# Optimization experiments

Hardware: AMD Instinct MI355X
Metric: run time of the kernel (lower is better)

## Reference

```python
import jax, jax.numpy as jnp
import numpy as np

NY, NX = 2048, 2048
DX = 5.0
DT = 0.8
BETA = 4.0
RHO = 1.0 / 9.81
EPS_ETA = 0.001
MANNING2 = 0.055 ** 2
PAD = ((0, 0), (0, 0), (1, 1), (1, 1))


def _conv3(x, w):
    # 1-channel 3x3 stencil, VALID padding: [1,1,H+2,W+2] -> [1,1,H,W]
    return jax.lax.conv_general_dilated(
        x, w, window_strides=(1, 1), padding='VALID',
        dimension_numbers=('NCHW', 'OIHW', 'NCHW'))


def _bc_u(u):
    # zero left/right columns, copy top/bottom rows (free-slip in y, no-flow in x)
    p = jnp.pad(u, PAD)
    p = p.at[:, :, 0, :].set(p[:, :, 1, :])
    p = p.at[:, :, -1, :].set(p[:, :, -2, :])
    return p


def _bc_v(v):
    # copy left/right columns, zero top/bottom rows
    p = jnp.pad(v, PAD)
    p = p.at[:, :, :, 0].set(p[:, :, :, 1])
    p = p.at[:, :, :, -1].set(p[:, :, :, -2])
    return p


def _bc_eta(h):
    # Neumann (copy) on all four sides; column copies first, then rows (matches torch order)
    p = jnp.pad(h, PAD)
    p = p.at[:, :, :, -1].set(p[:, :, :, -2])
    p = p.at[:, :, :, 0].set(p[:, :, :, 1])
    p = p.at[:, :, -1, :].set(p[:, :, -2, :])
    p = p.at[:, :, 0, :].set(p[:, :, 1, :])
    return p


def _k_pg(wpad, u, v, w1, w2, w3):
    # Petrov-Galerkin dissipation coefficient
    amp = 0.5 * (jnp.abs(u) + jnp.abs(v)) / DX  # = 1/2 dx^-2 (|u|dx + |v|dx)
    num = 0.25 * DX * jnp.abs(amp * _conv3(wpad, w1))
    den = EPS_ETA + 0.5 * (jnp.abs(_conv3(wpad, w2)) + jnp.abs(_conv3(wpad, w3))) / DX ** 2
    return num / den


def _pg_vector(uu, vv, u, v, k3, w1, w2, w3):
    k_u = _k_pg(uu, u, v, w1, w2, w3)
    k_v = _k_pg(vv, u, v, w1, w2, w3)
    k_uu = jnp.pad(jnp.minimum(k_u, k3), PAD)
    k_vv = jnp.pad(jnp.minimum(k_v, k3), PAD)
    k_x = 0.5 * (k_u * _conv3(uu, w1) + _conv3(uu * k_uu, w1) - u * _conv3(k_uu, w1))
    k_y = 0.5 * (k_v * _conv3(vv, w1) + _conv3(vv * k_vv, w1) - v * _conv3(k_vv, w1))
    return k_x, k_y


def _pg_scalar(hh, h, u, v, k3, w1, w2, w3):
    k_u = _k_pg(hh, u, v, w1, w2, w3)
    k_uu = jnp.pad(jnp.minimum(k_u, k3), PAD)
    return 0.5 * (k_u * _conv3(hh, w1) + _conv3(hh * k_uu, w1) - h * _conv3(k_uu, w1))


def _forward(values_u, values_v, values_H, values_h, k1, k2, k3,
             source_h, dif_values_h, values_hh, w1, w2, w3, wm):
    diag = -w1[0, 0, 1, 1]
    uu = _bc_u(values_u)
    vv = _bc_v(values_v)
    k_x, k_y = _pg_vector(uu, vv, values_u, values_v, k3, w1, w2, w3)
    hp = _bc_eta(values_h)
    # predictor (half) step
    b_u = (k_x * DT - values_u * _conv3(uu, w2) * DT - values_v * _conv3(uu, w3) * DT) * 0.5 + values_u
    b_v = (k_y * DT - values_u * _conv3(vv, w2) * DT - values_v * _conv3(vv, w3) * DT) * 0.5 + values_v
    b_u = b_u - _conv3(hp, w2) * DT
    b_v = b_v - _conv3(hp, w3) * DT
    b_uu = _bc_u(b_u)  # note: padded fields built BEFORE friction division, as in source
    b_vv = _bc_v(b_v)
    depth43 = jnp.maximum(k1, values_H + values_h) ** (4.0 / 3.0)
    sigma_q = jnp.sqrt(b_u ** 2 + b_v ** 2) * MANNING2 / depth43
    b_u = b_u / (1.0 + sigma_q * DT / RHO)
    b_v = b_v / (1.0 + sigma_q * DT / RHO)
    # corrector (full) step
    k_x, k_y = _pg_vector(b_uu, b_vv, b_u, b_v, k3, w1, w2, w3)
    u_n = values_u + k_x * DT - b_u * _conv3(b_uu, w2) * DT - b_v * _conv3(b_uu, w3) * DT
    v_n = values_v + k_y * DT - b_u * _conv3(b_vv, w2) * DT - b_v * _conv3(b_vv, w3) * DT
    u_n = u_n - _conv3(hp, w2) * DT
    v_n = v_n - _conv3(hp, w3) * DT
    sigma_q = jnp.sqrt(u_n ** 2 + v_n ** 2) * MANNING2 / depth43
    u_n = u_n / (1.0 + sigma_q * DT / RHO)
    v_n = v_n / (1.0 + sigma_q * DT / RHO)
    uu = _bc_u(u_n)
    vv = _bc_v(v_n)
    eta1 = jnp.maximum(k2, values_H + values_h)
    eta2 = jnp.maximum(k1, values_H + values_h)
    e1p = _bc_eta(eta1)
    b = BETA * RHO * (
        -_conv3(e1p, w2) * u_n - _conv3(e1p, w3) * v_n
        - eta1 * _conv3(uu, w2) - eta1 * _conv3(vv, w3)
        + _pg_scalar(e1p, eta1, u_n, v_n, k3, w1, w2, w3)
        - _conv3(_bc_eta(dif_values_h), wm) / DT
        + source_h) / (DT * eta2)
    # two Jacobi iterations for the wave (pressure) equation
    coef = BETA * RHO / (DT ** 2 * eta2)
    denom = diag + coef
    hh = values_hh
    for _ in range(2):
        hh = hh - (-_conv3(_bc_eta(hh), w1) + coef * hh) / denom + b / denom
    h_new = values_h + hh
    dif_h = h_new - values_h
    hhp = _bc_eta(hh)
    u_n = u_n - _conv3(hhp, w2) * DT / RHO
    v_n = v_n - _conv3(hhp, w3) * DT / RHO
    return (u_n, v_n, h_new, hh, b, dif_h)


def setup_inputs() -> dict:
    key = jax.random.key(0)
    k = jax.random.split(key, 6)
    shape = (1, 1, NY, NX)
    w1 = jnp.asarray(np.array([[1, 1, 1], [1, -8, 1], [1, 1, 1]], np.float32) / 3.0 / DX ** 2).reshape(1, 1, 3, 3)
    w2 = jnp.asarray(np.array([[-1, 0, 1], [-4, 0, 4], [-1, 0, 1]], np.float32) / 12.0 / DX).reshape(1, 1, 3, 3)
    w3 = jnp.transpose(w2, (0, 1, 3, 2))
    wm = jnp.asarray(np.array([[1, 4, 1], [4, 16, 4], [1, 4, 1]], np.float32) / 36.0).reshape(1, 1, 3, 3)
    return {
        'values_u': jax.random.normal(k[0], shape, jnp.float32) * 0.5,
        'values_v': jax.random.normal(k[1], shape, jnp.float32) * 0.5,
        'values_H': jax.random.uniform(k[2], shape, jnp.float32) * 10.0,  # bathymetric depth
        'values_h': jax.random.normal(k[3], shape, jnp.float32) * 0.1,   # free-surface elevation
        'k1': jnp.full(shape, EPS_ETA, jnp.float32),
        'k2': jnp.zeros(shape, jnp.float32),
        'k3': jnp.full(shape, DX ** 2 * 0.1 / DT, jnp.float32),
        'source_h': jax.random.normal(k[4], shape, jnp.float32) * 0.01,
        'dif_values_h': jax.random.normal(k[5], shape, jnp.float32) * 0.01,
        'values_hh': jnp.zeros(shape, jnp.float32),
        'w1': w1, 'w2': w2, 'w3': w3, 'wm': wm,
    }


def reference(values_u, values_v, values_H, values_h, k1, k2, k3,
              source_h, dif_values_h, values_hh, w1, w2, w3, wm):
    return _forward(values_u, values_v, values_H, values_h, k1, k2, k3,
                    source_h, dif_values_h, values_hh, w1, w2, w3, wm)
```

## Files before the change

kernel.cpp:

```cpp
#include <hip/hip_runtime.h>
#include <math.h>


#define NY 2048
#define NX 2048

#define BX 32
#define BY 8
#define SW (BX + 4)
#define KW (BX + 2)

#define DXf   5.0f
#define DTf   0.8f
#define EPSf  0.001f
#define K3f   3.125f
__device__ __constant__ float M2f   = (float)(0.055 * 0.055);
__device__ __constant__ float RHOf  = (float)(1.0 / 9.81);
__device__ __constant__ float BRf   = (float)(4.0 / 9.81);
__device__ __constant__ float DT2f  = (float)(0.8 * 0.8);
__device__ __constant__ float C43f  = (float)(4.0 / 3.0);

#define W1E ((1.0f / 3.0f) / 25.0f)
#define W1C ((-8.0f / 3.0f) / 25.0f)
#define DIAGf ((8.0f / 3.0f) / 25.0f)
#define W2A ((1.0f / 12.0f) / 5.0f)
#define W2B ((4.0f / 12.0f) / 5.0f)
#define WMA (1.0f / 36.0f)
#define WMB (4.0f / 36.0f)
#define WMC (16.0f / 36.0f)

__device__ __forceinline__ int iclamp(int v, int lo, int hi) {
    return v < lo ? lo : (v > hi ? hi : v);
}

__device__ __forceinline__ float uuAt(const float* __restrict__ u, int y, int x) {
    if ((unsigned)x >= (unsigned)NX) return 0.0f;
    y = iclamp(y, 0, NY - 1);
    return u[y * NX + x];
}
__device__ __forceinline__ float vvAt(const float* __restrict__ v, int y, int x) {
    if ((unsigned)y >= (unsigned)NY) return 0.0f;
    x = iclamp(x, 0, NX - 1);
    return v[y * NX + x];
}
__device__ __forceinline__ float etaAt(const float* __restrict__ h, int y, int x) {
    y = iclamp(y, 0, NY - 1);
    x = iclamp(x, 0, NX - 1);
    return h[y * NX + x];
}

__device__ __forceinline__ float cW1(const float* s, int st) {
    float nb = s[-st - 1] + s[-st] + s[-st + 1] + s[-1] + s[1] + s[st - 1] + s[st] + s[st + 1];
    return W1E * nb + W1C * s[0];
}
__device__ __forceinline__ float cW2(const float* s, int st) {
    return W2A * ((s[-st + 1] - s[-st - 1]) + (s[st + 1] - s[st - 1])) + W2B * (s[1] - s[-1]);
}
__device__ __forceinline__ float cW3(const float* s, int st) {
    return W2A * ((s[st - 1] - s[-st - 1]) + (s[st + 1] - s[-st + 1])) + W2B * (s[st] - s[-st]);
}

__device__ __forceinline__ float kpg(float uq, float vq, float c1, float c2, float c3) {
    float amp = (0.5f * (fabsf(uq) + fabsf(vq))) / DXf;
    float num = 1.25f * fabsf(amp * c1);
    float den = EPSf + (0.5f * (fabsf(c2) + fabsf(c3))) / 25.0f;
    return num / den;
}

__device__ __forceinline__ float prodW1(const float* pf, const float* pk) {
    float nb = pf[-SW - 1] * pk[-KW - 1] + pf[-SW] * pk[-KW] + pf[-SW + 1] * pk[-KW + 1]
             + pf[-1] * pk[-1] + pf[1] * pk[1]
             + pf[SW - 1] * pk[KW - 1] + pf[SW] * pk[KW] + pf[SW + 1] * pk[KW + 1];
    return W1E * nb + W1C * (pf[0] * pk[0]);
}

__global__ __launch_bounds__(256)
void kA(const float* __restrict__ u, const float* __restrict__ v,
        const float* __restrict__ H, const float* __restrict__ h,
        float* __restrict__ bupre, float* __restrict__ bvpre,
        float* __restrict__ d43o, float* __restrict__ buo, float* __restrict__ bvo)
{
    const int tx0 = blockIdx.x * BX, ty0 = blockIdx.y * BY;
    const int lx = threadIdx.x, ly = threadIdx.y, tid = ly * BX + lx;
    __shared__ float su[BY + 4][SW], sv[BY + 4][SW], sh[BY + 2][KW];
    __shared__ float sku[BY + 2][KW], skum[BY + 2][KW], skv[BY + 2][KW], skvm[BY + 2][KW];

    for (int t = tid; t < (BY + 4) * SW; t += 256) {
        int r = t / SW, c = t % SW;
        int gy = ty0 + r - 2, gx = tx0 + c - 2;
        su[r][c] = uuAt(u, gy, gx);
        sv[r][c] = vvAt(v, gy, gx);
    }
    for (int t = tid; t < (BY + 2) * KW; t += 256) {
        int r = t / KW, c = t % KW;
        sh[r][c] = etaAt(h, ty0 + r - 1, tx0 + c - 1);
    }
    __syncthreads();

    for (int t = tid; t < (BY + 2) * KW; t += 256) {
        int r = t / KW, c = t % KW;
        int gy = ty0 + r - 1, gx = tx0 + c - 1;
        float ku = 0.f, kum = 0.f, kv = 0.f, kvm = 0.f;
        if ((unsigned)gy < (unsigned)NY && (unsigned)gx < (unsigned)NX) {
            const float* pu = &su[r + 1][c + 1];
            const float* pv = &sv[r + 1][c + 1];
            float uq = pu[0], vq = pv[0];
            ku = kpg(uq, vq, cW1(pu, SW), cW2(pu, SW), cW3(pu, SW));
            kum = fminf(ku, K3f);
            kv = kpg(uq, vq, cW1(pv, SW), cW2(pv, SW), cW3(pv, SW));
            kvm = fminf(kv, K3f);
        }
        sku[r][c] = ku; skum[r][c] = kum; skv[r][c] = kv; skvm[r][c] = kvm;
    }
    __syncthreads();

    const int y = ty0 + ly, x = tx0 + lx, idx = y * NX + x;
    const float* pu = &su[ly + 2][lx + 2];
    const float* pv = &sv[ly + 2][lx + 2];
    const float* ph = &sh[ly + 1][lx + 1];
    const float* pum = &skum[ly + 1][lx + 1];
    const float* pvm = &skvm[ly + 1][lx + 1];
    float uc = pu[0], vc = pv[0];

    float kx = 0.5f * (sku[ly + 1][lx + 1] * cW1(pu, SW) + prodW1(pu, pum) - uc * cW1(pum, KW));
    float ky = 0.5f * (skv[ly + 1][lx + 1] * cW1(pv, SW) + prodW1(pv, pvm) - vc * cW1(pvm, KW));

    float cw2u = cW2(pu, SW), cw3u = cW3(pu, SW);
    float cw2v = cW2(pv, SW), cw3v = cW3(pv, SW);
    float cw2h = cW2(ph, KW), cw3h = cW3(ph, KW);

    float bu = (kx * DTf - uc * cw2u * DTf - vc * cw3u * DTf) * 0.5f + uc;
    bu = bu - cw2h * DTf;
    float bv = (ky * DTf - uc * cw2v * DTf - vc * cw3v * DTf) * 0.5f + vc;
    bv = bv - cw3h * DTf;

    float dep = fmaxf(EPSf, H[idx] + ph[0]);
    float d43 = powf(dep, C43f);
    float sq = sqrtf(bu * bu + bv * bv) * M2f / d43;
    float fr = 1.0f + (sq * DTf) / RHOf;

    bupre[idx] = bu;
    bvpre[idx] = bv;
    d43o[idx] = d43;
    buo[idx] = bu / fr;
    bvo[idx] = bv / fr;
}

__global__ __launch_bounds__(256)
void kB(const float* __restrict__ u, const float* __restrict__ v, const float* __restrict__ h,
        const float* __restrict__ bupre, const float* __restrict__ bvpre,
        const float* __restrict__ bupost, const float* __restrict__ bvpost,
        const float* __restrict__ d43, float* __restrict__ uno, float* __restrict__ vno)
{
    const int tx0 = blockIdx.x * BX, ty0 = blockIdx.y * BY;
    const int lx = threadIdx.x, ly = threadIdx.y, tid = ly * BX + lx;
    __shared__ float su[BY + 4][SW], sv[BY + 4][SW], sh[BY + 2][KW];
    __shared__ float sku[BY + 2][KW], skum[BY + 2][KW], skv[BY + 2][KW], skvm[BY + 2][KW];

    for (int t = tid; t < (BY + 4) * SW; t += 256) {
        int r = t / SW, c = t % SW;
        int gy = ty0 + r - 2, gx = tx0 + c - 2;
        su[r][c] = uuAt(bupre, gy, gx);
        sv[r][c] = vvAt(bvpre, gy, gx);
    }
    for (int t = tid; t < (BY + 2) * KW; t += 256) {
        int r = t / KW, c = t % KW;
        sh[r][c] = etaAt(h, ty0 + r - 1, tx0 + c - 1);
    }
    __syncthreads();

    for (int t = tid; t < (BY + 2) * KW; t += 256) {
        int r = t / KW, c = t % KW;
        int gy = ty0 + r - 1, gx = tx0 + c - 1;
        float ku = 0.f, kum = 0.f, kv = 0.f, kvm = 0.f;
        if ((unsigned)gy < (unsigned)NY && (unsigned)gx < (unsigned)NX) {
            const float* pu = &su[r + 1][c + 1];
            const float* pv = &sv[r + 1][c + 1];
            float uq = bupost[gy * NX + gx], vq = bvpost[gy * NX + gx];
            ku = kpg(uq, vq, cW1(pu, SW), cW2(pu, SW), cW3(pu, SW));
            kum = fminf(ku, K3f);
            kv = kpg(uq, vq, cW1(pv, SW), cW2(pv, SW), cW3(pv, SW));
            kvm = fminf(kv, K3f);
        }
        sku[r][c] = ku; skum[r][c] = kum; skv[r][c] = kv; skvm[r][c] = kvm;
    }
    __syncthreads();

    const int y = ty0 + ly, x = tx0 + lx, idx = y * NX + x;
    const float* pu = &su[ly + 2][lx + 2];
    const float* pv = &sv[ly + 2][lx + 2];
    const float* ph = &sh[ly + 1][lx + 1];
    const float* pum = &skum[ly + 1][lx + 1];
    const float* pvm = &skvm[ly + 1][lx + 1];
    float buc = bupost[idx], bvc = bvpost[idx];

    float kx = 0.5f * (sku[ly + 1][lx + 1] * cW1(pu, SW) + prodW1(pu, pum) - buc * cW1(pum, KW));
    float ky = 0.5f * (skv[ly + 1][lx + 1] * cW1(pv, SW) + prodW1(pv, pvm) - bvc * cW1(pvm, KW));

    float un = u[idx] + kx * DTf - buc * cW2(pu, SW) * DTf - bvc * cW3(pu, SW) * DTf;
    un = un - cW2(ph, KW) * DTf;
    float vn = v[idx] + ky * DTf - buc * cW2(pv, SW) * DTf - bvc * cW3(pv, SW) * DTf;
    vn = vn - cW3(ph, KW) * DTf;

    float d = d43[idx];
    float sq = sqrtf(un * un + vn * vn) * M2f / d;
    float fr = 1.0f + (sq * DTf) / RHOf;
    uno[idx] = un / fr;
    vno[idx] = vn / fr;
}

__global__ __launch_bounds__(256)
void kC(const float* __restrict__ H, const float* __restrict__ h,
        const float* __restrict__ un, const float* __restrict__ vn,
        const float* __restrict__ dif, const float* __restrict__ src,
        const float* __restrict__ hh0,
        float* __restrict__ bo, float* __restrict__ hh1o)
{
    const int tx0 = blockIdx.x * BX, ty0 = blockIdx.y * BY;
    const int lx = threadIdx.x, ly = threadIdx.y, tid = ly * BX + lx;
    __shared__ float se[BY + 4][SW], sh0[BY + 2][KW];
    __shared__ float sks[BY + 2][KW], sksm[BY + 2][KW];

    for (int t = tid; t < (BY + 4) * SW; t += 256) {
        int r = t / SW, c = t % SW;
        int cy = iclamp(ty0 + r - 2, 0, NY - 1), cx = iclamp(tx0 + c - 2, 0, NX - 1);
        se[r][c] = fmaxf(0.0f, H[cy * NX + cx] + h[cy * NX + cx]);
    }
    for (int t = tid; t < (BY + 2) * KW; t += 256) {
        int r = t / KW, c = t % KW;
        sh0[r][c] = etaAt(hh0, ty0 + r - 1, tx0 + c - 1);
    }
    __syncthreads();

    for (int t = tid; t < (BY + 2) * KW; t += 256) {
        int r = t / KW, c = t % KW;
        int gy = ty0 + r - 1, gx = tx0 + c - 1;
        float ks = 0.f, ksm = 0.f;
        if ((unsigned)gy < (unsigned)NY && (unsigned)gx < (unsigned)NX) {
            const float* pe = &se[r + 1][c + 1];
            float uq = un[gy * NX + gx], vq = vn[gy * NX + gx];
            ks = kpg(uq, vq, cW1(pe, SW), cW2(pe, SW), cW3(pe, SW));
            ksm = fminf(ks, K3f);
        }
        sks[r][c] = ks; sksm[r][c] = ksm;
    }
    __syncthreads();

    const int y = ty0 + ly, x = tx0 + lx, idx = y * NX + x;
    const float* pe = &se[ly + 2][lx + 2];
    const float* pk = &sksm[ly + 1][lx + 1];
    float e1c = pe[0];

    float pg = 0.5f * (sks[ly + 1][lx + 1] * cW1(pe, SW) + prodW1(pe, pk) - e1c * cW1(pk, KW));
    float cw2e = cW2(pe, SW), cw3e = cW3(pe, SW);
    float unc = un[idx], vnc = vn[idx];

    float cw2un = W2A * ((uuAt(un, y - 1, x + 1) - uuAt(un, y - 1, x - 1))
                       + (uuAt(un, y + 1, x + 1) - uuAt(un, y + 1, x - 1)))
                + W2B * (uuAt(un, y, x + 1) - uuAt(un, y, x - 1));
    float cw3vn = W2A * ((vvAt(vn, y + 1, x - 1) - vvAt(vn, y - 1, x - 1))
                       + (vvAt(vn, y + 1, x + 1) - vvAt(vn, y - 1, x + 1)))
                + W2B * (vvAt(vn, y + 1, x) - vvAt(vn, y - 1, x));
    float cwm = WMA * (etaAt(dif, y - 1, x - 1) + etaAt(dif, y - 1, x + 1)
                     + etaAt(dif, y + 1, x - 1) + etaAt(dif, y + 1, x + 1))
              + WMB * (etaAt(dif, y - 1, x) + etaAt(dif, y, x - 1)
                     + etaAt(dif, y, x + 1) + etaAt(dif, y + 1, x))
              + WMC * etaAt(dif, y, x);

    float eta2 = fmaxf(EPSf, H[idx] + h[idx]);
    float sum = -cw2e * unc - cw3e * vnc - e1c * cw2un - e1c * cw3vn + pg
                - cwm / DTf + src[idx];
    float b = (BRf * sum) / (DTf * eta2);
    float coef = BRf / (DT2f * eta2);
    float dn = DIAGf + coef;

    const float* p0 = &sh0[ly + 1][lx + 1];
    float hc = p0[0];
    float cv = cW1(p0, KW);
    float hh1 = hc - (-cv + coef * hc) / dn + b / dn;

    bo[idx] = b;
    hh1o[idx] = hh1;
}

__global__ __launch_bounds__(256)
void kD(const float* __restrict__ H, const float* __restrict__ h,
        const float* __restrict__ un, const float* __restrict__ vn,
        const float* __restrict__ b, const float* __restrict__ hh1,
        float* __restrict__ o_u, float* __restrict__ o_v, float* __restrict__ o_h,
        float* __restrict__ o_hh, float* __restrict__ o_dif)
{
    const int tx0 = blockIdx.x * BX, ty0 = blockIdx.y * BY;
    const int lx = threadIdx.x, ly = threadIdx.y, tid = ly * BX + lx;
    __shared__ float s1[BY + 4][SW];
    __shared__ float s2[BY + 2][KW];

    for (int t = tid; t < (BY + 4) * SW; t += 256) {
        int r = t / SW, c = t % SW;
        s1[r][c] = etaAt(hh1, ty0 + r - 2, tx0 + c - 2);
    }
    __syncthreads();

    for (int t = tid; t < (BY + 2) * KW; t += 256) {
        int r = t / KW, c = t % KW;
        int cy = iclamp(ty0 + r - 1, 0, NY - 1), cx = iclamp(tx0 + c - 1, 0, NX - 1);
        const float* p = &s1[cy - ty0 + 2][cx - tx0 + 2];
        float hc = p[0];
        float cv = cW1(p, SW);
        int gi = cy * NX + cx;
        float coef = BRf / (DT2f * fmaxf(EPSf, H[gi] + h[gi]));
        float dn = DIAGf + coef;
        s2[r][c] = hc - (-cv + coef * hc) / dn + b[gi] / dn;
    }
    __syncthreads();

    const int y = ty0 + ly, x = tx0 + lx, idx = y * NX + x;
    const float* p2 = &s2[ly + 1][lx + 1];
    float hh2 = p2[0];
    float hcen = h[idx];
    float hnew = hcen + hh2;

    float cw2 = cW2(p2, KW), cw3 = cW3(p2, KW);

    o_u[idx] = un[idx] - (cw2 * DTf) / RHOf;
    o_v[idx] = vn[idx] - (cw3 * DTf) / RHOf;
    o_h[idx] = hnew;
    o_hh[idx] = hh2;
    o_dif[idx] = hnew - hcen;
}

extern "C" void kernel_launch(void* const* d_in, const int* in_sizes, int n_in,
                              void* d_out, int out_size, void* d_ws, size_t ws_size,
                              hipStream_t stream)
{
    const float* u   = (const float*)d_in[0];
    const float* v   = (const float*)d_in[1];
    const float* H   = (const float*)d_in[2];
    const float* h   = (const float*)d_in[3];
    const float* src = (const float*)d_in[7];
    const float* dif = (const float*)d_in[8];
    const float* hh0 = (const float*)d_in[9];

    float* out = (float*)d_out;
    const size_t N = (size_t)NY * NX;
    float* o0 = out;
    float* o1 = out + N;
    float* o2 = out + 2 * N;
    float* o3 = out + 3 * N;
    float* o4 = out + 4 * N;
    float* o5 = out + 5 * N;

    float* ws  = (float*)d_ws;
    float* un  = ws;
    float* vn  = ws + N;
    float* hh1 = ws + 2 * N;

    dim3 blk(BX, BY);
    dim3 grd(NX / BX, NY / BY);

    kA<<<grd, blk, 0, stream>>>(u, v, H, h, o0, o1, o2, o3, o4);
    kB<<<grd, blk, 0, stream>>>(u, v, h, o0, o1, o3, o4, o2, un, vn);
    kC<<<grd, blk, 0, stream>>>(H, h, un, vn, dif, src, hh0, o4, hh1);
    kD<<<grd, blk, 0, stream>>>(H, h, un, vn, o4, hh1, o0, o1, o2, o3, o5);
}
```

Measured before the change: 423.3 us.

## Widen tiles, cache stencil results in shared memory, use fast reciprocal math

Tile width doubles to 64 (512 threads per block), and halo loads become 2D strided loops with no integer division. The first-pass stencil results (cW1/cW2/cW3) are stored in shared memory so the second pass reuses them instead of recomputing. In kC, the un/vn/dif neighbourhoods are staged through shared memory rather than read from global memory nine times each. Divisions, powf and sqrtf are replaced with AMD rcp/log/exp2/sqrt intrinsics plus one Newton step, which can change precision slightly and raises shared memory use per block.

```diff
diff --git a/kernel.cpp b/kernel.cpp
--- a/kernel.cpp
+++ b/kernel.cpp
@@ -5,20 +5,26 @@
 #define NY 2048
 #define NX 2048
 
-#define BX 32
+#define BX 64
 #define BY 8
-#define SW (BX + 4)
+#define TH (BY + 4)
+#define TW (BX + 4)
+#define KH (BY + 2)
 #define KW (BX + 2)
 
 #define DXf   5.0f
 #define DTf   0.8f
 #define EPSf  0.001f
 #define K3f   3.125f
-__device__ __constant__ float M2f   = (float)(0.055 * 0.055);
-__device__ __constant__ float RHOf  = (float)(1.0 / 9.81);
-__device__ __constant__ float BRf   = (float)(4.0 / 9.81);
-__device__ __constant__ float DT2f  = (float)(0.8 * 0.8);
-__device__ __constant__ float C43f  = (float)(4.0 / 3.0);
+
+__device__ constexpr float M2f    = (float)(0.055 * 0.055);
+__device__ constexpr float RHO_   = (float)(1.0 / 9.81);
+__device__ constexpr float BRf    = (float)(4.0 / 9.81);
+__device__ constexpr float DT2f   = (float)(0.8 * 0.8);
+__device__ constexpr float C43f   = (float)(4.0 / 3.0);
+__device__ constexpr float DTRHO  = 0.8f / RHO_;
+__device__ constexpr float INVDT  = 1.0f / 0.8f;
+__device__ constexpr float CBRDT2 = BRf / DT2f;
 
 #define W1E ((1.0f / 3.0f) / 25.0f)
 #define W1C ((-8.0f / 3.0f) / 25.0f)
@@ -33,6 +39,11 @@
     return v < lo ? lo : (v > hi ? hi : v);
 }
 
+__device__ __forceinline__ float frcp(float x) {
+    float r = __builtin_amdgcn_rcpf(x);
+    return r * (2.0f - x * r);
+}
+
 __device__ __forceinline__ float uuAt(const float* __restrict__ u, int y, int x) {
     if ((unsigned)x >= (unsigned)NX) return 0.0f;
     y = iclamp(y, 0, NY - 1);
@@ -49,68 +60,86 @@
     return h[y * NX + x];
 }
 
-__device__ __forceinline__ float cW1(const float* s, int st) {
-    float nb = s[-st - 1] + s[-st] + s[-st + 1] + s[-1] + s[1] + s[st - 1] + s[st] + s[st + 1];
+template<int ST>
+__device__ __forceinline__ float cw1f(const float* s) {
+    float nb = s[-ST - 1] + s[-ST] + s[-ST + 1] + s[-1] + s[1] + s[ST - 1] + s[ST] + s[ST + 1];
     return W1E * nb + W1C * s[0];
 }
-__device__ __forceinline__ float cW2(const float* s, int st) {
-    return W2A * ((s[-st + 1] - s[-st - 1]) + (s[st + 1] - s[st - 1])) + W2B * (s[1] - s[-1]);
-}
-__device__ __forceinline__ float cW3(const float* s, int st) {
-    return W2A * ((s[st - 1] - s[-st - 1]) + (s[st + 1] - s[-st + 1])) + W2B * (s[st] - s[-st]);
-}
-
-__device__ __forceinline__ float kpg(float uq, float vq, float c1, float c2, float c3) {
-    float amp = (0.5f * (fabsf(uq) + fabsf(vq))) / DXf;
+template<int ST>
+__device__ __forceinline__ float cw2f(const float* s) {
+    return W2A * ((s[-ST + 1] - s[-ST - 1]) + (s[ST + 1] - s[ST - 1])) + W2B * (s[1] - s[-1]);
+}
+template<int ST>
+__device__ __forceinline__ float cw3f(const float* s) {
+    return W2A * ((s[ST - 1] - s[-ST - 1]) + (s[ST + 1] - s[-ST + 1])) + W2B * (s[ST] - s[-ST]);
+}
+
+__device__ __forceinline__ float kpgf(float uq, float vq, float c1, float c2, float c3) {
+    float amp = 0.5f * (fabsf(uq) + fabsf(vq)) * 0.2f;
     float num = 1.25f * fabsf(amp * c1);
-    float den = EPSf + (0.5f * (fabsf(c2) + fabsf(c3))) / 25.0f;
-    return num / den;
-}
-
-__device__ __forceinline__ float prodW1(const float* pf, const float* pk) {
-    float nb = pf[-SW - 1] * pk[-KW - 1] + pf[-SW] * pk[-KW] + pf[-SW + 1] * pk[-KW + 1]
-             + pf[-1] * pk[-1] + pf[1] * pk[1]
-             + pf[SW - 1] * pk[KW - 1] + pf[SW] * pk[KW] + pf[SW + 1] * pk[KW + 1];
-    return W1E * nb + W1C * (pf[0] * pk[0]);
-}
-
-__global__ __launch_bounds__(256)
+    float den = EPSf + 0.5f * (fabsf(c2) + fabsf(c3)) * 0.04f;
+    return num * frcp(den);
+}
+
+template<int FS, int KS>
+__device__ __forceinline__ void prod_and_k(const float* pf, const float* pk,
+                                           float& prodw1, float& kw1) {
+    float k0 = pk[-KS - 1], k1 = pk[-KS], k2 = pk[-KS + 1], k3 = pk[-1], kc = pk[0],
+          k4 = pk[1], k5 = pk[KS - 1], k6 = pk[KS], k7 = pk[KS + 1];
+    float nbk = k0 + k1 + k2 + k3 + k4 + k5 + k6 + k7;
+    float nbp = pf[-FS - 1] * k0 + pf[-FS] * k1 + pf[-FS + 1] * k2 + pf[-1] * k3
+              + pf[1] * k4 + pf[FS - 1] * k5 + pf[FS] * k6 + pf[FS + 1] * k7;
+    kw1 = W1E * nbk + W1C * kc;
+    prodw1 = W1E * nbp + W1C * (pf[0] * kc);
+}
+
+__global__ __launch_bounds__(512)
 void kA(const float* __restrict__ u, const float* __restrict__ v,
         const float* __restrict__ H, const float* __restrict__ h,
         float* __restrict__ bupre, float* __restrict__ bvpre,
         float* __restrict__ d43o, float* __restrict__ buo, float* __restrict__ bvo)
 {
     const int tx0 = blockIdx.x * BX, ty0 = blockIdx.y * BY;
-    const int lx = threadIdx.x, ly = threadIdx.y, tid = ly * BX + lx;
-    __shared__ float su[BY + 4][SW], sv[BY + 4][SW], sh[BY + 2][KW];
-    __shared__ float sku[BY + 2][KW], skum[BY + 2][KW], skv[BY + 2][KW], skvm[BY + 2][KW];
-
-    for (int t = tid; t < (BY + 4) * SW; t += 256) {
-        int r = t / SW, c = t % SW;
-        int gy = ty0 + r - 2, gx = tx0 + c - 2;
-        su[r][c] = uuAt(u, gy, gx);
-        sv[r][c] = vvAt(v, gy, gx);
-    }
-    for (int t = tid; t < (BY + 2) * KW; t += 256) {
-        int r = t / KW, c = t % KW;
-        sh[r][c] = etaAt(h, ty0 + r - 1, tx0 + c - 1);
-    }
-    __syncthreads();
-
-    for (int t = tid; t < (BY + 2) * KW; t += 256) {
-        int r = t / KW, c = t % KW;
-        int gy = ty0 + r - 1, gx = tx0 + c - 1;
-        float ku = 0.f, kum = 0.f, kv = 0.f, kvm = 0.f;
-        if ((unsigned)gy < (unsigned)NY && (unsigned)gx < (unsigned)NX) {
+    const int lx = threadIdx.x, ly = threadIdx.y;
+    __shared__ float su[TH][TW], sv[TH][TW], sh[KH][KW];
+    __shared__ float sku[KH][KW], skum[KH][KW], skv[KH][KW], skvm[KH][KW];
+    __shared__ float c1u[KH][KW], c2u[KH][KW], c3u[KH][KW];
+    __shared__ float c1v[KH][KW], c2v[KH][KW], c3v[KH][KW];
+
+    for (int r = ly; r < TH; r += BY) {
+        int gy = ty0 + r - 2;
+        for (int c = lx; c < TW; c += BX) {
+            int gx = tx0 + c - 2;
+            su[r][c] = uuAt(u, gy, gx);
+            sv[r][c] = vvAt(v, gy, gx);
+        }
+    }
+    for (int r = ly; r < KH; r += BY) {
+        int gy = ty0 + r - 1;
+        for (int c = lx; c < KW; c += BX)
+            sh[r][c] = etaAt(h, gy, tx0 + c - 1);
+    }
+    __syncthreads();
+
+    for (int r = ly; r < KH; r += BY) {
+        int gy = ty0 + r - 1;
+        for (int c = lx; c < KW; c += BX) {
+            int gx = tx0 + c - 1;
             const float* pu = &su[r + 1][c + 1];
             const float* pv = &sv[r + 1][c + 1];
-            float uq = pu[0], vq = pv[0];
-            ku = kpg(uq, vq, cW1(pu, SW), cW2(pu, SW), cW3(pu, SW));
-            kum = fminf(ku, K3f);
-            kv = kpg(uq, vq, cW1(pv, SW), cW2(pv, SW), cW3(pv, SW));
-            kvm = fminf(kv, K3f);
-        }
-        sku[r][c] = ku; skum[r][c] = kum; skv[r][c] = kv; skvm[r][c] = kvm;
+            float a1 = cw1f<TW>(pu), a2 = cw2f<TW>(pu), a3 = cw3f<TW>(pu);
+            float b1 = cw1f<TW>(pv), b2 = cw2f<TW>(pv), b3 = cw3f<TW>(pv);
+            c1u[r][c] = a1; c2u[r][c] = a2; c3u[r][c] = a3;
+            c1v[r][c] = b1; c2v[r][c] = b2; c3v[r][c] = b3;
+            float ku = 0.f, kv = 0.f;
+            if ((unsigned)gy < (unsigned)NY && (unsigned)gx < (unsigned)NX) {
+                float uq = pu[0], vq = pv[0];
+                ku = kpgf(uq, vq, a1, a2, a3);
+                kv = kpgf(uq, vq, b1, b2, b3);
+            }
+            sku[r][c] = ku; skum[r][c] = fminf(ku, K3f);
+            skv[r][c] = kv; skvm[r][c] = fminf(kv, K3f);
+        }
     }
     __syncthreads();
 
@@ -118,71 +147,81 @@
     const float* pu = &su[ly + 2][lx + 2];
     const float* pv = &sv[ly + 2][lx + 2];
     const float* ph = &sh[ly + 1][lx + 1];
-    const float* pum = &skum[ly + 1][lx + 1];
-    const float* pvm = &skvm[ly + 1][lx + 1];
     float uc = pu[0], vc = pv[0];
 
-    float kx = 0.5f * (sku[ly + 1][lx + 1] * cW1(pu, SW) + prodW1(pu, pum) - uc * cW1(pum, KW));
-    float ky = 0.5f * (skv[ly + 1][lx + 1] * cW1(pv, SW) + prodW1(pv, pvm) - vc * cW1(pvm, KW));
-
-    float cw2u = cW2(pu, SW), cw3u = cW3(pu, SW);
-    float cw2v = cW2(pv, SW), cw3v = cW3(pv, SW);
-    float cw2h = cW2(ph, KW), cw3h = cW3(ph, KW);
-
-    float bu = (kx * DTf - uc * cw2u * DTf - vc * cw3u * DTf) * 0.5f + uc;
+    float pwu, kwu, pwv, kwv;
+    prod_and_k<TW, KW>(pu, &skum[ly + 1][lx + 1], pwu, kwu);
+    prod_and_k<TW, KW>(pv, &skvm[ly + 1][lx + 1], pwv, kwv);
+    float kx = 0.5f * (sku[ly + 1][lx + 1] * c1u[ly + 1][lx + 1] + pwu - uc * kwu);
+    float ky = 0.5f * (skv[ly + 1][lx + 1] * c1v[ly + 1][lx + 1] + pwv - vc * kwv);
+
+    float cw2h = cw2f<KW>(ph), cw3h = cw3f<KW>(ph);
+
+    float bu = (kx * DTf - uc * c2u[ly + 1][lx + 1] * DTf - vc * c3u[ly + 1][lx + 1] * DTf) * 0.5f + uc;
     bu = bu - cw2h * DTf;
-    float bv = (ky * DTf - uc * cw2v * DTf - vc * cw3v * DTf) * 0.5f + vc;
+    float bv = (ky * DTf - uc * c2v[ly + 1][lx + 1] * DTf - vc * c3v[ly + 1][lx + 1] * DTf) * 0.5f + vc;
     bv = bv - cw3h * DTf;
 
     float dep = fmaxf(EPSf, H[idx] + ph[0]);
-    float d43 = powf(dep, C43f);
-    float sq = sqrtf(bu * bu + bv * bv) * M2f / d43;
-    float fr = 1.0f + (sq * DTf) / RHOf;
+    float d43 = __builtin_amdgcn_exp2f(C43f * __builtin_amdgcn_logf(dep));
+    float sq = __builtin_amdgcn_sqrtf(bu * bu + bv * bv) * M2f * frcp(d43);
+    float rf = frcp(1.0f + sq * DTRHO);
 
     bupre[idx] = bu;
     bvpre[idx] = bv;
     d43o[idx] = d43;
-    buo[idx] = bu / fr;
-    bvo[idx] = bv / fr;
-}
-
-__global__ __launch_bounds__(256)
+    buo[idx] = bu * rf;
+    bvo[idx] = bv * rf;
+}
+
+__global__ __launch_bounds__(512)
 void kB(const float* __restrict__ u, const float* __restrict__ v, const float* __restrict__ h,
         const float* __restrict__ bupre, const float* __restrict__ bvpre,
         const float* __restrict__ bupost, const float* __restrict__ bvpost,
         const float* __restrict__ d43, float* __restrict__ uno, float* __restrict__ vno)
 {
     const int tx0 = blockIdx.x * BX, ty0 = blockIdx.y * BY;
-    const int lx = threadIdx.x, ly = threadIdx.y, tid = ly * BX + lx;
-    __shared__ float su[BY + 4][SW], sv[BY + 4][SW], sh[BY + 2][KW];
-    __shared__ float sku[BY + 2][KW], skum[BY + 2][KW], skv[BY + 2][KW], skvm[BY + 2][KW];
-
-    for (int t = tid; t < (BY + 4) * SW; t += 256) {
-        int r = t / SW, c = t % SW;
-        int gy = ty0 + r - 2, gx = tx0 + c - 2;
-        su[r][c] = uuAt(bupre, gy, gx);
-        sv[r][c] = vvAt(bvpre, gy, gx);
-    }
-    for (int t = tid; t < (BY + 2) * KW; t += 256) {
-        int r = t / KW, c = t % KW;
-        sh[r][c] = etaAt(h, ty0 + r - 1, tx0 + c - 1);
-    }
-    __syncthreads();
-
-    for (int t = tid; t < (BY + 2) * KW; t += 256) {
-        int r = t / KW, c = t % KW;
-        int gy = ty0 + r - 1, gx = tx0 + c - 1;
-        float ku = 0.f, kum = 0.f, kv = 0.f, kvm = 0.f;
-        if ((unsigned)gy < (unsigned)NY && (unsigned)gx < (unsigned)NX) {
+    const int lx = threadIdx.x, ly = threadIdx.y;
+    __shared__ float su[TH][TW], sv[TH][TW], sh[KH][KW];
+    __shared__ float sku[KH][KW], skum[KH][KW], skv[KH][KW], skvm[KH][KW];
+    __shared__ float c1u[KH][KW], c2u[KH][KW], c3u[KH][KW];
+    __shared__ float c1v[KH][KW], c2v[KH][KW], c3v[KH][KW];
+
+    for (int r = ly; r < TH; r += BY) {
+        int gy = ty0 + r - 2;
+        for (int c = lx; c < TW; c += BX) {
+            int gx = tx0 + c - 2;
+            su[r][c] = uuAt(bupre, gy, gx);
+            sv[r][c] = vvAt(bvpre, gy, gx);
+        }
+    }
+    for (int r = ly; r < KH; r += BY) {
+        int gy = ty0 + r - 1;
+        for (int c = lx; c < KW; c += BX)
+            sh[r][c] = etaAt(h, gy, tx0 + c - 1);
+    }
+    __syncthreads();
+
+    for (int r = ly; r < KH; r += BY) {
+        int gy = ty0 + r - 1;
+        for (int c = lx; c < KW; c += BX) {
+            int gx = tx0 + c - 1;
             const float* pu = &su[r + 1][c + 1];
             const float* pv = &sv[r + 1][c + 1];
-            float uq = bupost[gy * NX + gx], vq = bvpost[gy * NX + gx];
-            ku = kpg(uq, vq, cW1(pu, SW), cW2(pu, SW), cW3(pu, SW));
-            kum = fminf(ku, K3f);
-            kv = kpg(uq, vq, cW1(pv, SW), cW2(pv, SW), cW3(pv, SW));
-            kvm = fminf(kv, K3f);
-        }
-        sku[r][c] = ku; skum[r][c] = kum; skv[r][c] = kv; skvm[r][c] = kvm;
+            float a1 = cw1f<TW>(pu), a2 = cw2f<TW>(pu), a3 = cw3f<TW>(pu);
+            float b1 = cw1f<TW>(pv), b2 = cw2f<TW>(pv), b3 = cw3f<TW>(pv);
+            c1u[r][c] = a1; c2u[r][c] = a2; c3u[r][c] = a3;
+            c1v[r][c] = b1; c2v[r][c] = b2; c3v[r][c] = b3;
+            float ku = 0.f, kv = 0.f;
+            if ((unsigned)gy < (unsigned)NY && (unsigned)gx < (unsigned)NX) {
+                int gi = gy * NX + gx;
+                float uq = bupost[gi], vq = bvpost[gi];
+                ku = kpgf(uq, vq, a1, a2, a3);
+                kv = kpgf(uq, vq, b1, b2, b3);
+            }
+            sku[r][c] = ku; skum[r][c] = fminf(ku, K3f);
+            skv[r][c] = kv; skvm[r][c] = fminf(kv, K3f);
+        }
     }
     __syncthreads();
 
@@ -190,26 +229,26 @@
     const float* pu = &su[ly + 2][lx + 2];
     const float* pv = &sv[ly + 2][lx + 2];
     const float* ph = &sh[ly + 1][lx + 1];
-    const float* pum = &skum[ly + 1][lx + 1];
-    const float* pvm = &skvm[ly + 1][lx + 1];
     float buc = bupost[idx], bvc = bvpost[idx];
 
-    float kx = 0.5f * (sku[ly + 1][lx + 1] * cW1(pu, SW) + prodW1(pu, pum) - buc * cW1(pum, KW));
-    float ky = 0.5f * (skv[ly + 1][lx + 1] * cW1(pv, SW) + prodW1(pv, pvm) - bvc * cW1(pvm, KW));
-
-    float un = u[idx] + kx * DTf - buc * cW2(pu, SW) * DTf - bvc * cW3(pu, SW) * DTf;
-    un = un - cW2(ph, KW) * DTf;
-    float vn = v[idx] + ky * DTf - buc * cW2(pv, SW) * DTf - bvc * cW3(pv, SW) * DTf;
-    vn = vn - cW3(ph, KW) * DTf;
-
-    float d = d43[idx];
-    float sq = sqrtf(un * un + vn * vn) * M2f / d;
-    float fr = 1.0f + (sq * DTf) / RHOf;
-    uno[idx] = un / fr;
-    vno[idx] = vn / fr;
-}
-
-__global__ __launch_bounds__(256)
+    float pwu, kwu, pwv, kwv;
+    prod_and_k<TW, KW>(pu, &skum[ly + 1][lx + 1], pwu, kwu);
+    prod_and_k<TW, KW>(pv, &skvm[ly + 1][lx + 1], pwv, kwv);
+    float kx = 0.5f * (sku[ly + 1][lx + 1] * c1u[ly + 1][lx + 1] + pwu - buc * kwu);
+    float ky = 0.5f * (skv[ly + 1][lx + 1] * c1v[ly + 1][lx + 1] + pwv - bvc * kwv);
+
+    float un = u[idx] + kx * DTf - buc * c2u[ly + 1][lx + 1] * DTf - bvc * c3u[ly + 1][lx + 1] * DTf;
+    un = un - cw2f<KW>(ph) * DTf;
+    float vn = v[idx] + ky * DTf - buc * c2v[ly + 1][lx + 1] * DTf - bvc * c3v[ly + 1][lx + 1] * DTf;
+    vn = vn - cw3f<KW>(ph) * DTf;
+
+    float sq = __builtin_amdgcn_sqrtf(un * un + vn * vn) * M2f * frcp(d43[idx]);
+    float rf = frcp(1.0f + sq * DTRHO);
+    uno[idx] = un * rf;
+    vno[idx] = vn * rf;
+}
+
+__global__ __launch_bounds__(512)
 void kC(const float* __restrict__ H, const float* __restrict__ h,
         const float* __restrict__ un, const float* __restrict__ vn,
         const float* __restrict__ dif, const float* __restrict__ src,
@@ -217,73 +256,84 @@
         float* __restrict__ bo, float* __restrict__ hh1o)
 {
     const int tx0 = blockIdx.x * BX, ty0 = blockIdx.y * BY;
-    const int lx = threadIdx.x, ly = threadIdx.y, tid = ly * BX + lx;
-    __shared__ float se[BY + 4][SW], sh0[BY + 2][KW];
-    __shared__ float sks[BY + 2][KW], sksm[BY + 2][KW];
-
-    for (int t = tid; t < (BY + 4) * SW; t += 256) {
-        int r = t / SW, c = t % SW;
-        int cy = iclamp(ty0 + r - 2, 0, NY - 1), cx = iclamp(tx0 + c - 2, 0, NX - 1);
-        se[r][c] = fmaxf(0.0f, H[cy * NX + cx] + h[cy * NX + cx]);
-    }
-    for (int t = tid; t < (BY + 2) * KW; t += 256) {
-        int r = t / KW, c = t % KW;
-        sh0[r][c] = etaAt(hh0, ty0 + r - 1, tx0 + c - 1);
-    }
-    __syncthreads();
-
-    for (int t = tid; t < (BY + 2) * KW; t += 256) {
-        int r = t / KW, c = t % KW;
-        int gy = ty0 + r - 1, gx = tx0 + c - 1;
-        float ks = 0.f, ksm = 0.f;
-        if ((unsigned)gy < (unsigned)NY && (unsigned)gx < (unsigned)NX) {
+    const int lx = threadIdx.x, ly = threadIdx.y;
+    __shared__ float se[TH][TW], sh0[KH][KW];
+    __shared__ float sun[KH][KW], svn[KH][KW], sdif[KH][KW];
+    __shared__ float sks[KH][KW], sksm[KH][KW];
+    __shared__ float c1e[KH][KW], c2e[KH][KW], c3e[KH][KW];
+
+    for (int r = ly; r < TH; r += BY) {
+        int gy = ty0 + r - 2;
+        for (int c = lx; c < TW; c += BX) {
+            int gx = tx0 + c - 2;
+            int cy = iclamp(gy, 0, NY - 1), cx = iclamp(gx, 0, NX - 1);
+            int gi = cy * NX + cx;
+            se[r][c] = fmaxf(0.0f, H[gi] + h[gi]);
+        }
+    }
+    for (int r = ly; r < KH; r += BY) {
+        int gy = ty0 + r - 1;
+        for (int c = lx; c < KW; c += BX) {
+            int gx = tx0 + c - 1;
+            sh0[r][c]  = etaAt(hh0, gy, gx);
+            sun[r][c]  = uuAt(un, gy, gx);
+            svn[r][c]  = vvAt(vn, gy, gx);
+            sdif[r][c] = etaAt(dif, gy, gx);
+        }
+    }
+    __syncthreads();
+
+    for (int r = ly; r < KH; r += BY) {
+        int gy = ty0 + r - 1;
+        for (int c = lx; c < KW; c += BX) {
+            int gx = tx0 + c - 1;
             const float* pe = &se[r + 1][c + 1];
-            float uq = un[gy * NX + gx], vq = vn[gy * NX + gx];
-            ks = kpg(uq, vq, cW1(pe, SW), cW2(pe, SW), cW3(pe, SW));
-            ksm = fminf(ks, K3f);
-        }
-        sks[r][c] = ks; sksm[r][c] = ksm;
+            float a1 = cw1f<TW>(pe), a2 = cw2f<TW>(pe), a3 = cw3f<TW>(pe);
+            c1e[r][c] = a1; c2e[r][c] = a2; c3e[r][c] = a3;
+            float ks = 0.f;
+            if ((unsigned)gy < (unsigned)NY && (unsigned)gx < (unsigned)NX)
+                ks = kpgf(sun[r][c], svn[r][c], a1, a2, a3);
+            sks[r][c] = ks; sksm[r][c] = fminf(ks, K3f);
+        }
     }
     __syncthreads();
 
     const int y = ty0 + ly, x = tx0 + lx, idx = y * NX + x;
     const float* pe = &se[ly + 2][lx + 2];
-    const float* pk = &sksm[ly + 1][lx + 1];
     float e1c = pe[0];
 
-    float pg = 0.5f * (sks[ly + 1][lx + 1] * cW1(pe, SW) + prodW1(pe, pk) - e1c * cW1(pk, KW));
-    float cw2e = cW2(pe, SW), cw3e = cW3(pe, SW);
-    float unc = un[idx], vnc = vn[idx];
-
-    float cw2un = W2A * ((uuAt(un, y - 1, x + 1) - uuAt(un, y - 1, x - 1))
-                       + (uuAt(un, y + 1, x + 1) - uuAt(un, y + 1, x - 1)))
-                + W2B * (uuAt(un, y, x + 1) - uuAt(un, y, x - 1));
-    float cw3vn = W2A * ((vvAt(vn, y + 1, x - 1) - vvAt(vn, y - 1, x - 1))
-                       + (vvAt(vn, y + 1, x + 1) - vvAt(vn, y - 1, x + 1)))
-                + W2B * (vvAt(vn, y + 1, x) - vvAt(vn, y - 1, x));
-    float cwm = WMA * (etaAt(dif, y - 1, x - 1) + etaAt(dif, y - 1, x + 1)
-                     + etaAt(dif, y + 1, x - 1) + etaAt(dif, y + 1, x + 1))
-              + WMB * (etaAt(dif, y - 1, x) + etaAt(dif, y, x - 1)
-                     + etaAt(dif, y, x + 1) + etaAt(dif, y + 1, x))
-              + WMC * etaAt(dif, y, x);
+    float pw, kw;
+    prod_and_k<TW, KW>(pe, &sksm[ly + 1][lx + 1], pw, kw);
+    float pg = 0.5f * (sks[ly + 1][lx + 1] * c1e[ly + 1][lx + 1] + pw - e1c * kw);
+
+    const float* psu = &sun[ly + 1][lx + 1];
+    const float* psv = &svn[ly + 1][lx + 1];
+    const float* pd  = &sdif[ly + 1][lx + 1];
+    float unc = psu[0], vnc = psv[0];
+    float cw2un = cw2f<KW>(psu);
+    float cw3vn = cw3f<KW>(psv);
+    float cwm = WMA * (pd[-KW - 1] + pd[-KW + 1] + pd[KW - 1] + pd[KW + 1])
+              + WMB * (pd[-KW] + pd[-1] + pd[1] + pd[KW])
+              + WMC * pd[0];
 
     float eta2 = fmaxf(EPSf, H[idx] + h[idx]);
-    float sum = -cw2e * unc - cw3e * vnc - e1c * cw2un - e1c * cw3vn + pg
-                - cwm / DTf + src[idx];
-    float b = (BRf * sum) / (DTf * eta2);
-    float coef = BRf / (DT2f * eta2);
-    float dn = DIAGf + coef;
+    float sum = -c2e[ly + 1][lx + 1] * unc - c3e[ly + 1][lx + 1] * vnc
+              - e1c * cw2un - e1c * cw3vn + pg - cwm * INVDT + src[idx];
+    float re2 = frcp(eta2);
+    float b = (BRf * sum) * INVDT * re2;
+    float coef = CBRDT2 * re2;
+    float rdn = frcp(DIAGf + coef);
 
     const float* p0 = &sh0[ly + 1][lx + 1];
     float hc = p0[0];
-    float cv = cW1(p0, KW);
-    float hh1 = hc - (-cv + coef * hc) / dn + b / dn;
+    float cv = cw1f<KW>(p0);
+    float hh1 = hc + (cv - coef * hc) * rdn + b * rdn;
 
     bo[idx] = b;
     hh1o[idx] = hh1;
 }
 
-__global__ __launch_bounds__(256)
+__global__ __launch_bounds__(512)
 void kD(const float* __restrict__ H, const float* __restrict__ h,
         const float* __restrict__ un, const float* __restrict__ vn,
         const float* __restrict__ b, const float* __restrict__ hh1,
@@ -291,26 +341,29 @@
         float* __restrict__ o_hh, float* __restrict__ o_dif)
 {
     const int tx0 = blockIdx.x * BX, ty0 = blockIdx.y * BY;
-    const int lx = threadIdx.x, ly = threadIdx.y, tid = ly * BX + lx;
-    __shared__ float s1[BY + 4][SW];
-    __shared__ float s2[BY + 2][KW];
-
-    for (int t = tid; t < (BY + 4) * SW; t += 256) {
-        int r = t / SW, c = t % SW;
-        s1[r][c] = etaAt(hh1, ty0 + r - 2, tx0 + c - 2);
-    }
-    __syncthreads();
-
-    for (int t = tid; t < (BY + 2) * KW; t += 256) {
-        int r = t / KW, c = t % KW;
-        int cy = iclamp(ty0 + r - 1, 0, NY - 1), cx = iclamp(tx0 + c - 1, 0, NX - 1);
-        const float* p = &s1[cy - ty0 + 2][cx - tx0 + 2];
-        float hc = p[0];
-        float cv = cW1(p, SW);
-        int gi = cy * NX + cx;
-        float coef = BRf / (DT2f * fmaxf(EPSf, H[gi] + h[gi]));
-        float dn = DIAGf + coef;
-        s2[r][c] = hc - (-cv + coef * hc) / dn + b[gi] / dn;
+    const int lx = threadIdx.x, ly = threadIdx.y;
+    __shared__ float s1[TH][TW];
+    __shared__ float s2[KH][KW];
+
+    for (int r = ly; r < TH; r += BY) {
+        int gy = ty0 + r - 2;
+        for (int c = lx; c < TW; c += BX)
+            s1[r][c] = etaAt(hh1, gy, tx0 + c - 2);
+    }
+    __syncthreads();
+
+    for (int r = ly; r < KH; r += BY) {
+        int cy = iclamp(ty0 + r - 1, 0, NY - 1);
+        for (int c = lx; c < KW; c += BX) {
+            int cx = iclamp(tx0 + c - 1, 0, NX - 1);
+            const float* p = &s1[cy - ty0 + 2][cx - tx0 + 2];
+            float hc = p[0];
+            float cv = cw1f<TW>(p);
+            int gi = cy * NX + cx;
+            float coef = CBRDT2 * frcp(fmaxf(EPSf, H[gi] + h[gi]));
+            float rdn = frcp(DIAGf + coef);
+            s2[r][c] = hc + (cv - coef * hc) * rdn + b[gi] * rdn;
+        }
     }
     __syncthreads();
 
@@ -320,10 +373,8 @@
     float hcen = h[idx];
     float hnew = hcen + hh2;
 
-    float cw2 = cW2(p2, KW), cw3 = cW3(p2, KW);
-
-    o_u[idx] = un[idx] - (cw2 * DTf) / RHOf;
-    o_v[idx] = vn[idx] - (cw3 * DTf) / RHOf;
+    o_u[idx] = un[idx] - cw2f<KW>(p2) * DTRHO;
+    o_v[idx] = vn[idx] - cw3f<KW>(p2) * DTRHO;
     o_h[idx] = hnew;
     o_hh[idx] = hh2;
     o_dif[idx] = hnew - hcen;
```

After: 460.2 us. 8.7% more time.
